# Optimization experiments

Measured on AMD Instinct MI355X. Metric: run time of the kernel, lower is better.

The kernel has to match this reference:

```python
import jax, jax.numpy as jnp
import numpy as np

B, L, C, H = 8, 2048, 256, 4
D = C // H  # head_dim = 64
EPS = 1e-5


def setup_inputs() -> dict:
    key = jax.random.key(0)
    ks = jax.random.split(key, 16)
    s = lambda fan_in: 1.0 / np.sqrt(fan_in)
    inp = {
        'x0': jax.random.normal(ks[0], (B, L, C), jnp.float32),
        'x1': jax.random.normal(ks[1], (B, L, C), jnp.float32),
        # attention projections (stored as (in, out); torch Linear is x @ W.T + b)
        'Wqk': jax.random.normal(ks[2], (C, C), jnp.float32) * s(C),
        'bqk': jax.random.normal(ks[3], (C,), jnp.float32) * s(C),
        'Wv': jax.random.normal(ks[4], (C, C), jnp.float32) * s(C),
        'bv': jax.random.normal(ks[5], (C,), jnp.float32) * s(C),
        'Wout': jax.random.normal(ks[6], (C, C), jnp.float32) * s(C),
        'bout': jax.random.normal(ks[7], (C,), jnp.float32) * s(C),
        # shared FFN: Linear(2C->2C) -> LayerNorm -> GELU -> Linear(2C->C)
        'W1': jax.random.normal(ks[8], (2 * C, 2 * C), jnp.float32) * s(2 * C),
        'b1': jax.random.normal(ks[9], (2 * C,), jnp.float32) * s(2 * C),
        'ln_g': jnp.ones((2 * C,), jnp.float32),
        'ln_b': jnp.zeros((2 * C,), jnp.float32),
        'W2': jax.random.normal(ks[10], (2 * C, C), jnp.float32) * s(2 * C),
        'b2': jax.random.normal(ks[11], (C,), jnp.float32) * s(2 * C),
    }
    return inp


def _heads(t):
    # (B, L, C) -> (B, H, L, D)
    b, l, _ = t.shape
    return t.reshape(b, l, H, D).transpose(0, 2, 1, 3)


def _merge(t):
    # (B, H, L, D) -> (B, L, C)
    b, h, l, d = t.shape
    return t.transpose(0, 2, 1, 3).reshape(b, l, h * d)


def _ffn(z, W1, b1, ln_g, ln_b, W2, b2):
    h = z @ W1 + b1
    mu = jnp.mean(h, axis=-1, keepdims=True)
    var = jnp.var(h, axis=-1, keepdims=True)
    h = (h - mu) * jax.lax.rsqrt(var + EPS) * ln_g + ln_b
    h = jax.nn.gelu(h, approximate=False)
    return h @ W2 + b2


def reference(x0, x1, Wqk, bqk, Wv, bv, Wout, bout, W1, b1, ln_g, ln_b, W2, b2):
    scale_sqrt = D ** (-0.25)  # sqrt(head_dim**-0.5), applied to both sides
    qk0 = _heads(x0 @ Wqk + bqk) * scale_sqrt  # (B,H,M,D)
    qk1 = _heads(x1 @ Wqk + bqk) * scale_sqrt  # (B,H,N,D)
    v0 = _heads(x0 @ Wv + bv)
    v1 = _heads(x1 @ Wv + bv)

    # single shared similarity matrix (LightGlue trick)
    sim = jnp.einsum('bhid,bhjd->bhij', qk0, qk1)  # (B,H,M,N)
    attn01 = jax.nn.softmax(sim, axis=-1)           # rows: A->B
    attn10 = jax.nn.softmax(sim, axis=-2)           # cols: B->A (softmax of sim^T along last dim)
    m0 = jnp.einsum('bhij,bhjd->bhid', attn01, v1)  # (B,H,M,D)
    m1 = jnp.einsum('bhij,bhid->bhjd', attn10, v0)  # (B,H,N,D)

    m0 = _merge(m0) @ Wout + bout
    m1 = _merge(m1) @ Wout + bout

    x0_out = x0 + _ffn(jnp.concatenate([x0, m0], axis=-1), W1, b1, ln_g, ln_b, W2, b2)
    x1_out = x1 + _ffn(jnp.concatenate([x1, m1], axis=-1), W1, b1, ln_g, ln_b, W2, b2)
    return (x0_out, x1_out)
```

## Files before the change

### kernel.cpp

```cpp
#include <hip/hip_runtime.h>
#include <hip/hip_bf16.h>

typedef _Float16 f16;
typedef _Float16 f16x8 __attribute__((ext_vector_type(8)));
typedef _Float16 f16x4 __attribute__((ext_vector_type(4)));
typedef _Float16 f16x2 __attribute__((ext_vector_type(2)));
typedef float f32x4 __attribute__((ext_vector_type(4)));
typedef float f32x2 __attribute__((ext_vector_type(2)));

#define MFMA16(a, b, c) __builtin_amdgcn_mfma_f32_16x16x32_f16((a), (b), (c), 0, 0, 0)

__device__ __forceinline__ void load16(const void* g, void* l) {
    __builtin_amdgcn_global_load_lds((const __attribute__((address_space(1))) void*)g,
                                     (__attribute__((address_space(3))) void*)l, 16, 0, 0);
}

__device__ __forceinline__ unsigned int pkrtz(float a, float b) {
    return __builtin_bit_cast(unsigned int, __builtin_amdgcn_cvt_pkrtz(a, b));
}

__global__ __launch_bounds__(256) void k_prep(const float* __restrict__ x0,
                                              const float* __restrict__ x1,
                                              const float* __restrict__ Wqk,
                                              const float* __restrict__ Wv,
                                              const float* __restrict__ W1,
                                              const float* __restrict__ W2,
                                              const float* __restrict__ Wout,
                                              const float* __restrict__ b1,
                                              const float* __restrict__ bout,
                                              f16* __restrict__ xh, f16* __restrict__ wcat_t,
                                              f16* __restrict__ w1t, f16* __restrict__ w1bt,
                                              f16* __restrict__ w2t, f16* __restrict__ woutf16,
                                              float* __restrict__ bias_eff) {
    __shared__ float red[4];
    const int blk = blockIdx.x, tid = threadIdx.x;
    if (blk < 8192) {
        size_t i = ((size_t)blk * 256 + tid) * 4;
        const float* src = (i < 4194304) ? (x0 + i) : (x1 + (i - 4194304));
        float4 v = *(const float4*)src;
        f16x4 o = {(f16)v.x, (f16)v.y, (f16)v.z, (f16)v.w};
        *(f16x4*)(xh + i) = o;
    } else if (blk < 8704) {
        int n = blk - 8192;
        const float* W = (n < 256) ? Wqk : Wv;
        wcat_t[n * 256 + tid] = (f16)W[tid * 256 + (n & 255)];
    } else if (blk < 9216) {
        int n = blk - 8704;
        w1t[n * 512 + tid] = (f16)W1[tid * 512 + n];
    } else if (blk < 9728) {
        int n = blk - 9216;
        w1bt[n * 256 + tid] = (f16)W1[(256 + tid) * 512 + n];
    } else if (blk < 10240) {
        int j = blk - 9728;
        int n = j >> 1, k = (j & 1) * 256 + tid;
        w2t[n * 512 + k] = (f16)W2[k * 256 + n];
    } else if (blk < 10496) {
        int o = (blk - 10240) * 256 + tid;
        woutf16[o] = (f16)Wout[o];
    } else {
        int n = blk - 10496;
        float s = bout[tid] * W1[(size_t)(256 + tid) * 512 + n];
#pragma unroll
        for (int off = 1; off < 64; off <<= 1) s += __shfl_xor(s, off);
        int wave = tid >> 6, lane = tid & 63;
        if (lane == 0) red[wave] = s;
        __syncthreads();
        if (tid == 0) bias_eff[n] = b1[n] + red[0] + red[1] + red[2] + red[3];
    }
}

__global__ __launch_bounds__(256, 2) void k_gemm(const f16* __restrict__ A1,
                                                 const f16* __restrict__ A2, int ksplit,
                                                 int strideA, const f16* __restrict__ Bt, int K,
                                                 int N, const float* __restrict__ bias1,
                                                 const float* __restrict__ bias2, int mode,
                                                 void* __restrict__ out1, void* __restrict__ out2,
                                                 const f16* __restrict__ resh,
                                                 const f16* __restrict__ pgA,
                                                 const f16* __restrict__ pgBt,
                                                 f16* __restrict__ pgOut) {
    int bm0 = blockIdx.x * 128;
    int bn0 = blockIdx.y * 256;
    if (pgOut != nullptr && blockIdx.x >= 256) {
        if (blockIdx.y != 0) return;
        A1 = pgA;
        A2 = pgA;
        ksplit = 1 << 30;
        strideA = 256;
        Bt = pgBt;
        K = 256;
        N = 256;
        bias1 = nullptr;
        bias2 = nullptr;
        mode = 4;
        out1 = pgOut;
        out2 = nullptr;
        resh = nullptr;
        bm0 = (blockIdx.x - 256) * 128;
        bn0 = 0;
    }
    __shared__ f16 As[2][4096];
    __shared__ f16 Bs[2][8192];
    const int tid = threadIdx.x;
    const int lane = tid & 63, wave = tid >> 6;
    const int quad = lane >> 4, l16 = lane & 15;
    const int wm0 = (wave & 1) * 64, wn0 = (wave >> 1) * 128;
    const int axor = l16 & 3;

    f32x4 acc[4][8];
#pragma unroll
    for (int tm = 0; tm < 4; tm++)
#pragma unroll
        for (int tn = 0; tn < 8; tn++) acc[tm][tn] = (f32x4){0.f, 0.f, 0.f, 0.f};

    auto stage = [&](int buf, int kt) {
        const int k0 = kt * 32;
        const f16* Ab = (k0 < ksplit) ? A1 : A2;
        const int koff = (k0 < ksplit) ? k0 : k0 - ksplit;
#pragma unroll
        for (int rd = 0; rd < 2; rd++) {
            const int cbase = rd * 256 + wave * 64;
            const int c = cbase + lane;
            const int row = c >> 2, col = (c & 3) ^ (row & 3);
            load16(Ab + (size_t)(bm0 + row) * strideA + koff + col * 8, &As[buf][cbase * 8]);
        }
#pragma unroll
        for (int rd = 0; rd < 4; rd++) {
            const int cbase = rd * 256 + wave * 64;
            const int c = cbase + lane;
            const int row = c >> 2, col = (c & 3) ^ (row & 3);
            load16(Bt + (size_t)(bn0 + row) * K + k0 + col * 8, &Bs[buf][cbase * 8]);
        }
    };

    const int NT = K >> 5;
    stage(0, 0);
    __syncthreads();
    for (int kt = 0; kt < NT; kt++) {
        const int cur = kt & 1;
        if (kt + 1 < NT) stage(cur ^ 1, kt + 1);
        f16x8 af[4], bf[8];
#pragma unroll
        for (int t = 0; t < 4; t++)
            af[t] = *(const f16x8*)&As[cur][(wm0 + t * 16 + l16) * 32 + (quad ^ axor) * 8];
#pragma unroll
        for (int t = 0; t < 8; t++)
            bf[t] = *(const f16x8*)&Bs[cur][(wn0 + t * 16 + l16) * 32 + (quad ^ axor) * 8];
#pragma unroll
        for (int tm = 0; tm < 4; tm++)
#pragma unroll
            for (int tn = 0; tn < 8; tn++) acc[tm][tn] = MFMA16(bf[tn], af[tm], acc[tm][tn]);
        __syncthreads();
    }

    if (mode == 0 && bn0 == 0) {
        f16* tile = &Bs[0][0];
#pragma unroll
        for (int tm = 0; tm < 4; tm++) {
            const int r = (wave & 1) * 16 + l16;
#pragma unroll
            for (int tn = 0; tn < 8; tn++) {
                const int c = wn0 + tn * 16 + quad * 4;
                float4 bi = *(const float4*)(bias1 + c);
                f32x4 v = acc[tm][tn];
                f16x4 o = {(f16)((v[0] + bi.x) * 0.42466090f),
                           (f16)((v[1] + bi.y) * 0.42466090f),
                           (f16)((v[2] + bi.z) * 0.42466090f),
                           (f16)((v[3] + bi.w) * 0.42466090f)};
                *(f16x4*)&tile[r * 264 + c] = o;
            }
            __syncthreads();
#pragma unroll
            for (int j = 0; j < 4; j++) {
                const int ch = tid + j * 256;
                const int row = ch >> 5, cc = (ch & 31) * 8;
                const int m = bm0 + (row >> 4) * 64 + tm * 16 + (row & 15);
                const int s = m >> 14, r14 = m & 16383, b = r14 >> 11, l = r14 & 2047;
                const int h = cc >> 6, d = cc & 63;
                const size_t hh = (size_t)((s * 8 + b) * 4 + h);
                *(f16x8*)((f16*)out1 + (hh * 2048 + l) * 64 + d) =
                    *(const f16x8*)&tile[row * 264 + cc];
            }
            __syncthreads();
        }
        return;
    }

#pragma unroll
    for (int tm = 0; tm < 4; tm++) {
        const int m = bm0 + wm0 + tm * 16 + l16;
#pragma unroll
        for (int tn = 0; tn < 8; tn++) {
            const int n = bn0 + wn0 + tn * 16 + quad * 4;
            f32x4 v = acc[tm][tn];
            if (mode == 0) {
                const int s = m >> 14, r14 = m & 16383, b = r14 >> 11, l = r14 & 2047;
                const int n2 = n - 256;
                float4 bi = *(const float4*)(bias2 + n2);
                const int h = n2 >> 6, d = n2 & 63;
                const size_t hh = (size_t)((s * 8 + b) * 4 + h);
                f16* o2 = (f16*)out2 + (hh * 64 + d) * 2048 + l;
                o2[0] = (f16)(v[0] + bi.x);
                o2[2048] = (f16)(v[1] + bi.y);
                o2[4096] = (f16)(v[2] + bi.z);
                o2[6144] = (f16)(v[3] + bi.w);
            } else if (mode == 2) {
                float4 bi = *(const float4*)(bias1 + n);
                f16x4 o = {(f16)(v[0] + bi.x), (f16)(v[1] + bi.y), (f16)(v[2] + bi.z),
                           (f16)(v[3] + bi.w)};
                *(f16x4*)((f16*)out1 + (size_t)m * N + n) = o;
            } else if (mode == 3) {
                float4 bi = *(const float4*)(bias1 + n);
                f16x4 rr = *(const f16x4*)(resh + (size_t)m * 256 + n);
                float4 o = {v[0] + bi.x + (float)rr[0], v[1] + bi.y + (float)rr[1],
                            v[2] + bi.z + (float)rr[2], v[3] + bi.w + (float)rr[3]};
                *(float4*)((float*)out1 + (size_t)m * 256 + n) = o;
            } else {
                f16x4 o = {(f16)v[0], (f16)v[1], (f16)v[2], (f16)v[3]};
                *(f16x4*)((f16*)out1 + (size_t)m * 512 + 256 + n) = o;
            }
        }
    }
}

__global__ __launch_bounds__(256, 4) void k_flash(const f16* __restrict__ qkbuf,
                                                  const f16* __restrict__ vtbuf,
                                                  f16* __restrict__ mbuf) {
    const int z = blockIdx.z;
    const int bh = blockIdx.x;
    const int qt = blockIdx.y;
    const size_t HSZ = 2048 * 64;
    const size_t SSZ = 32 * HSZ;
    const f16* Q = qkbuf + (z ? SSZ : 0) + bh * HSZ;
    const f16* Kp = qkbuf + (z ? 0 : SSZ) + bh * HSZ;
    const f16* Vt = vtbuf + (z ? 0 : SSZ) + bh * HSZ;
    f16* Mo = mbuf + (size_t)z * (16384 * 256);

    __shared__ f16 Ks[2][4096];
    __shared__ f16 Vs[2][4096];

    const int tid = threadIdx.x, lane = tid & 63, wave = tid >> 6;
    const int quad = lane >> 4, l16 = lane & 15;
    const int srow = lane >> 3;
    const int slc = (lane & 7) ^ (srow & 7);
    const int sw = l16 & 7;

    const int q0 = qt * 128 + wave * 32;
    f16x8 qf[2][2];
#pragma unroll
    for (int tq = 0; tq < 2; tq++)
#pragma unroll
        for (int kk = 0; kk < 2; kk++)
            qf[tq][kk] =
                *(const f16x8*)(Q + (size_t)(q0 + tq * 16 + l16) * 64 + kk * 32 + quad * 8);

    const f16* kb[2] = {&Ks[0][l16 * 64 + ((0 + quad) ^ sw) * 8],
                        &Ks[0][l16 * 64 + ((4 + quad) ^ sw) * 8]};
    const f16* vb[2] = {&Vs[0][l16 * 64 + ((0 + quad) ^ sw) * 8],
                        &Vs[0][l16 * 64 + ((4 + quad) ^ sw) * 8]};

    const f16* pK0 = Kp + (size_t)(wave * 16 + srow) * 64 + slc * 8;
    const f16* pK1 = pK0 + 8 * 64;
    const f16* pV0 = Vt + (size_t)(wave * 16 + srow) * 2048 + slc * 8;
    const f16* pV1 = pV0 + 8 * 2048;
    f16* kd0 = &Ks[0][(wave * 2 + 0) * 512];
    f16* kd1 = &Ks[0][(wave * 2 + 1) * 512];
    f16* vd0 = &Vs[0][(wave * 2 + 0) * 512];
    f16* vd1 = &Vs[0][(wave * 2 + 1) * 512];

    auto stage = [&](int buf, int kv0) {
        load16(pK0 + (size_t)kv0 * 64, kd0 + buf * 4096);
        load16(pK1 + (size_t)kv0 * 64, kd1 + buf * 4096);
        load16(pV0 + kv0, vd0 + buf * 4096);
        load16(pV1 + kv0, vd1 + buf * 4096);
    };

    f32x4 oacc[4][2];
#pragma unroll
    for (int td = 0; td < 4; td++)
#pragma unroll
        for (int tq = 0; tq < 2; tq++) oacc[td][tq] = (f32x4){0.f, 0.f, 0.f, 0.f};
    f32x4 oext[2] = {{0.f, 0.f, 0.f, 0.f}, {0.f, 0.f, 0.f, 0.f}};
    const f16x8 vones = {(f16)1.f, (f16)1.f, (f16)1.f, (f16)1.f,
                         (f16)1.f, (f16)1.f, (f16)1.f, (f16)1.f};

    stage(0, 0);

    auto body = [&](int cur, int t) {
        if (t < 31) {
            stage(cur ^ 1, (t + 1) * 64);
            asm volatile("s_waitcnt vmcnt(4)" ::: "memory");
        } else {
            asm volatile("s_waitcnt vmcnt(0)" ::: "memory");
        }
        __builtin_amdgcn_s_barrier();

        f32x4 sacc[4][2];
#pragma unroll
        for (int tkv = 0; tkv < 4; tkv++)
#pragma unroll
            for (int tq = 0; tq < 2; tq++)
                sacc[tkv][tq] = (f32x4){-8.f, -8.f, -8.f, -8.f};
#pragma unroll
        for (int kk = 0; kk < 2; kk++) {
#pragma unroll
            for (int tkv = 0; tkv < 4; tkv++) {
                f16x8 ka = *(const f16x8*)(kb[kk] + cur * 4096 + tkv * 1024);
#pragma unroll
                for (int tq = 0; tq < 2; tq++)
                    sacc[tkv][tq] = MFMA16(ka, qf[tq][kk], sacc[tkv][tq]);
            }
        }

        f16x8 bfrag[2][2];
#pragma unroll
        for (int blk = 0; blk < 2; blk++) {
#pragma unroll
            for (int tq = 0; tq < 2; tq++) {
                unsigned int rg[2][2];
#pragma unroll
                for (int tt = 0; tt < 2; tt++) {
                    const int tkv = blk * 2 + tt;
                    float p0 = __builtin_amdgcn_exp2f(sacc[tkv][tq][0]);
                    float p1 = __builtin_amdgcn_exp2f(sacc[tkv][tq][1]);
                    float p2 = __builtin_amdgcn_exp2f(sacc[tkv][tq][2]);
                    float p3 = __builtin_amdgcn_exp2f(sacc[tkv][tq][3]);
                    rg[tt][0] = pkrtz(p0, p1);
                    rg[tt][1] = pkrtz(p2, p3);
                }
                auto ab0 = __builtin_amdgcn_permlane32_swap(rg[0][0], rg[1][0], false, false);
                auto uw0 = __builtin_amdgcn_permlane16_swap(ab0[0], ab0[1], false, false);
                auto ab1 = __builtin_amdgcn_permlane32_swap(rg[0][1], rg[1][1], false, false);
                auto uw1 = __builtin_amdgcn_permlane16_swap(ab1[0], ab1[1], false, false);
                union {
                    unsigned int u[4];
                    f16x8 v;
                } bb;
                bb.u[0] = uw0[0];
                bb.u[1] = uw1[0];
                bb.u[2] = uw0[1];
                bb.u[3] = uw1[1];
                bfrag[blk][tq] = bb.v;
            }
        }

#pragma unroll
        for (int blk = 0; blk < 2; blk++) {
#pragma unroll
            for (int td = 0; td < 4; td++) {
                f16x8 va = *(const f16x8*)(vb[blk] + cur * 4096 + td * 1024);
#pragma unroll
                for (int tq = 0; tq < 2; tq++)
                    oacc[td][tq] = MFMA16(va, bfrag[blk][tq], oacc[td][tq]);
            }
#pragma unroll
            for (int tq = 0; tq < 2; tq++)
                oext[tq] = MFMA16(vones, bfrag[blk][tq], oext[tq]);
        }
        __builtin_amdgcn_s_barrier();
    };

    for (int t = 0; t < 32; t += 2) {
        body(0, t);
        body(1, t + 1);
    }

    const int b = bh >> 2, h = bh & 3;
#pragma unroll
    for (int tq = 0; tq < 2; tq++) {
        const float inv = 1.f / oext[tq][0];
        const int q = q0 + tq * 16 + l16;
        const size_t base = ((size_t)(b * 2048 + q)) * 256 + h * 64;
#pragma unroll
        for (int td = 0; td < 4; td++) {
            f16x4 o = {(f16)(oacc[td][tq][0] * inv), (f16)(oacc[td][tq][1] * inv),
                       (f16)(oacc[td][tq][2] * inv), (f16)(oacc[td][tq][3] * inv)};
            *(f16x4*)(Mo + base + td * 16 + quad * 4) = o;
        }
    }
}

__global__ __launch_bounds__(256) void k_ln_gelu(f16* __restrict__ h,
                                                 const float* __restrict__ g,
                                                 const float* __restrict__ bb) {
    const int tid = threadIdx.x, wave = tid >> 6, lane = tid & 63;
    const size_t row = (size_t)blockIdx.x * 4 + wave;
    f16* hr = h + row * 512 + lane * 8;
    f16x8 v = *(const f16x8*)hr;
    float x[8];
    float s = 0.f, sq = 0.f;
#pragma unroll
    for (int i = 0; i < 8; i++) {
        x[i] = (float)v[i];
        s += x[i];
        sq += x[i] * x[i];
    }
#pragma unroll
    for (int off = 1; off < 64; off <<= 1) {
        s += __shfl_xor(s, off);
        sq += __shfl_xor(sq, off);
    }
    const float mu = s * (1.f / 512.f);
    const float var = sq * (1.f / 512.f) - mu * mu;
    const float rstd = rsqrtf(var + 1e-5f);
    float4 g0 = *(const float4*)(g + lane * 8), g1 = *(const float4*)(g + lane * 8 + 4);
    float4 b0 = *(const float4*)(bb + lane * 8), b1 = *(const float4*)(bb + lane * 8 + 4);
    float gg[8] = {g0.x, g0.y, g0.z, g0.w, g1.x, g1.y, g1.z, g1.w};
    float bv[8] = {b0.x, b0.y, b0.z, b0.w, b1.x, b1.y, b1.z, b1.w};
#pragma unroll
    for (int i = 0; i < 8; i++) {
        float a = (x[i] - mu) * rstd * gg[i] + bv[i];
        a = 0.5f * a * (1.f + erff(a * 0.70710678118f));
        v[i] = (f16)a;
    }
    *(f16x8*)hr = v;
}


extern "C" void kernel_launch(void* const* d_in, const int* in_sizes, int n_in, void* d_out,
                              int out_size, void* d_ws, size_t ws_size, hipStream_t stream) {
    const float* x0 = (const float*)d_in[0];
    const float* x1 = (const float*)d_in[1];
    const float* Wqk = (const float*)d_in[2];
    const float* bqk = (const float*)d_in[3];
    const float* Wv = (const float*)d_in[4];
    const float* bv = (const float*)d_in[5];
    const float* Wout = (const float*)d_in[6];
    const float* bout = (const float*)d_in[7];
    const float* W1 = (const float*)d_in[8];
    const float* b1 = (const float*)d_in[9];
    const float* lng = (const float*)d_in[10];
    const float* lnb = (const float*)d_in[11];
    const float* W2 = (const float*)d_in[12];
    const float* b2 = (const float*)d_in[13];
    float* out = (float*)d_out;

    char* ws = (char*)d_ws;
    f16* xh = (f16*)(ws);
    f16* qk = (f16*)(ws + 16777216);
    f16* vt = (f16*)(ws + 33554432);
    f16* mbuf = (f16*)(ws + 50331648);
    f16* hbuf = qk;
    f16* w1bt = (f16*)(ws + 50331648);
    f16* woutf16 = w1bt + 131072;
    f16* wcat_t = (f16*)(ws + 67108864);
    f16* w1t = wcat_t + 131072;
    f16* w2t = w1t + 262144;
    float* bias_eff = (float*)(w2t + 131072);

    k_prep<<<11008, 256, 0, stream>>>(x0, x1, Wqk, Wv, W1, W2, Wout, b1, bout, xh, wcat_t, w1t,
                                      w1bt, w2t, woutf16, bias_eff);
    k_gemm<<<dim3(260, 2), 256, 0, stream>>>(xh, xh, 1 << 30, 256, wcat_t, 256, 512, bqk, bv, 0,
                                             qk, vt, nullptr, w1bt, woutf16, w1t);
    k_flash<<<dim3(32, 16, 2), 256, 0, stream>>>(qk, vt, mbuf);
    k_gemm<<<dim3(256, 2), 256, 0, stream>>>(xh, mbuf, 256, 256, w1t, 512, 512, bias_eff,
                                             nullptr, 2, hbuf, nullptr, nullptr, nullptr,
                                             nullptr, nullptr);
    k_ln_gelu<<<8192, 256, 0, stream>>>(hbuf, lng, lnb);
    k_gemm<<<dim3(256, 1), 256, 0, stream>>>(hbuf, hbuf, 1 << 30, 512, w2t, 512, 256, b2,
                                             nullptr, 3, out, nullptr, xh, nullptr, nullptr,
                                             nullptr);
}
```

Before: 300.8 us.

## Use partial vmcnt waits in GEMM loop and stage mode 2/3 epilogues through LDS

The GEMM main loop now waits only for the previous stage's global-to-LDS loads (vmcnt(6)) before a raw barrier, instead of a full __syncthreads drain, so the next tile's prefetch stays in flight during compute. The mode 2 (f16 output) and mode 3 (f32 output plus residual) epilogues now stage accumulator tiles through LDS so global stores are wide and row-contiguous rather than scattered 4-element writes. The cost is extra LDS round-trips and barriers in the epilogue. Correctness depends on the hand-counted vmcnt matching the six outstanding loads per stage.

```diff
diff --git a/kernel.cpp b/kernel.cpp
--- a/kernel.cpp
+++ b/kernel.cpp
@@ -135,10 +135,15 @@
 
     const int NT = K >> 5;
     stage(0, 0);
-    __syncthreads();
     for (int kt = 0; kt < NT; kt++) {
         const int cur = kt & 1;
-        if (kt + 1 < NT) stage(cur ^ 1, kt + 1);
+        if (kt + 1 < NT) {
+            stage(cur ^ 1, kt + 1);
+            asm volatile("s_waitcnt vmcnt(6)" ::: "memory");
+        } else {
+            asm volatile("s_waitcnt vmcnt(0)" ::: "memory");
+        }
+        __builtin_amdgcn_s_barrier();
         f16x8 af[4], bf[8];
 #pragma unroll
         for (int t = 0; t < 4; t++)
@@ -150,7 +155,7 @@
         for (int tm = 0; tm < 4; tm++)
 #pragma unroll
             for (int tn = 0; tn < 8; tn++) acc[tm][tn] = MFMA16(bf[tn], af[tm], acc[tm][tn]);
-        __syncthreads();
+        __builtin_amdgcn_s_barrier();
     }
 
     if (mode == 0 && bn0 == 0) {
@@ -182,6 +187,68 @@
                     *(const f16x8*)&tile[row * 264 + cc];
             }
             __syncthreads();
+        }
+        return;
+    }
+
+    if (mode == 2) {
+        f16* tile = &Bs[0][0];
+#pragma unroll
+        for (int tm = 0; tm < 4; tm++) {
+            const int r = (wave & 1) * 16 + l16;
+#pragma unroll
+            for (int tn = 0; tn < 8; tn++) {
+                const int c = wn0 + tn * 16 + quad * 4;
+                float4 bi = *(const float4*)(bias1 + bn0 + c);
+                f32x4 v = acc[tm][tn];
+                f16x4 o = {(f16)(v[0] + bi.x), (f16)(v[1] + bi.y), (f16)(v[2] + bi.z),
+                           (f16)(v[3] + bi.w)};
+                *(f16x4*)&tile[r * 264 + c] = o;
+            }
+            __syncthreads();
+#pragma unroll
+            for (int j = 0; j < 4; j++) {
+                const int ch = tid + j * 256;
+                const int row = ch >> 5, cc = (ch & 31) * 8;
+                const int m = bm0 + (row >> 4) * 64 + tm * 16 + (row & 15);
+                *(f16x8*)((f16*)out1 + (size_t)m * N + bn0 + cc) =
+                    *(const f16x8*)&tile[row * 264 + cc];
+            }
+            __syncthreads();
+        }
+        return;
+    }
+
+    if (mode == 3) {
+        float* t32 = (float*)&Bs[0][0];
+#pragma unroll
+        for (int tm = 0; tm < 4; tm++) {
+#pragma unroll
+            for (int half = 0; half < 2; half++) {
+                if ((wave & 1) == half) {
+#pragma unroll
+                    for (int tn = 0; tn < 8; tn++) {
+                        const int c = wn0 + tn * 16 + quad * 4;
+                        float4 bi = *(const float4*)(bias1 + c);
+                        f32x4 v = acc[tm][tn];
+                        float4 o = {v[0] + bi.x, v[1] + bi.y, v[2] + bi.z, v[3] + bi.w};
+                        *(float4*)&t32[l16 * 264 + c] = o;
+                    }
+                }
+                __syncthreads();
+#pragma unroll
+                for (int j = 0; j < 4; j++) {
+                    const int ch = tid + j * 256;
+                    const int row = ch >> 6, cc = (ch & 63) * 4;
+                    const int m = bm0 + half * 64 + tm * 16 + row;
+                    f16x4 rr = *(const f16x4*)(resh + (size_t)m * 256 + cc);
+                    const float* ts = &t32[row * 264 + cc];
+                    float4 o = {ts[0] + (float)rr[0], ts[1] + (float)rr[1],
+                                ts[2] + (float)rr[2], ts[3] + (float)rr[3]};
+                    *(float4*)((float*)out1 + (size_t)m * 256 + cc) = o;
+                }
+                __syncthreads();
+            }
         }
         return;
     }
@@ -204,17 +271,6 @@
                 o2[2048] = (f16)(v[1] + bi.y);
                 o2[4096] = (f16)(v[2] + bi.z);
                 o2[6144] = (f16)(v[3] + bi.w);
-            } else if (mode == 2) {
-                float4 bi = *(const float4*)(bias1 + n);
-                f16x4 o = {(f16)(v[0] + bi.x), (f16)(v[1] + bi.y), (f16)(v[2] + bi.z),
-                           (f16)(v[3] + bi.w)};
-                *(f16x4*)((f16*)out1 + (size_t)m * N + n) = o;
-            } else if (mode == 3) {
-                float4 bi = *(const float4*)(bias1 + n);
-                f16x4 rr = *(const f16x4*)(resh + (size_t)m * 256 + n);
-                float4 o = {v[0] + bi.x + (float)rr[0], v[1] + bi.y + (float)rr[1],
-                            v[2] + bi.z + (float)rr[2], v[3] + bi.w + (float)rr[3]};
-                *(float4*)((float*)out1 + (size_t)m * 256 + n) = o;
             } else {
                 f16x4 o = {(f16)v[0], (f16)v[1], (f16)v[2], (f16)v[3]};
                 *(f16x4*)((f16*)out1 + (size_t)m * 512 + 256 + n) = o;
```

Result: no change. 296.3 us (-1.5%).
